# Performance work log

Measured on AMD Instinct MI355X. Metric: run time of the kernel, lower is better.

## Reference

```python
import jax, jax.numpy as jnp
import numpy as np

# SNN constants (standard STBP / quantized-SNN settings used in this style of repo)
THRESH = 0.5   # firing threshold
DECAY = 0.2    # membrane decay
LENS = 0.5     # surrogate-gradient window
QK = 4         # fractional bits for Quantize_Spike(0, 4) / QuantLinear

B, S = 128, 1024
VOCAB, EMB, EDIM, H = 50000, 100, 256, 1024  # H = 2 * num_hiddens


def _quant(x, lo, hi, k=QK):
    n = 2.0 ** k
    return jnp.clip(jnp.round(x * n) / n, lo, hi)


def quant_act(x):
    # Quantize_Spike(0, 4): 0 integer bits, 4 fractional bits, nonneg (post-ReLU)
    return _quant(x, 0.0, 1.0 - 2.0 ** (-QK))


def quant_w(w):
    # QuantLinear weight quantization, symmetric fixed-point
    return _quant(w, -(1.0 - 2.0 ** (-QK)), 1.0 - 2.0 ** (-QK))


def setup_inputs() -> dict:
    key = jax.random.key(0)
    ks = jax.random.split(key, 10)
    f = jnp.float32
    return {
        "inputs": jax.random.randint(ks[0], (B, S), 0, VOCAB),
        "emb": jax.random.normal(ks[1], (VOCAB, EMB), f) * 0.1,
        "W1": jax.random.normal(ks[2], (EDIM, EMB), f) * 0.1,
        "b1": jax.random.normal(ks[3], (EDIM,), f) * 0.01,
        "W2": jax.random.normal(ks[4], (H, EDIM), f) * 0.05,
        "b2": jax.random.normal(ks[5], (H,), f) * 0.01,
        "Wr2": jax.random.normal(ks[6], (H, H), f) * 0.02,
        "br2": jax.random.normal(ks[7], (H,), f) * 0.01,
        "W3": jax.random.normal(ks[8], (2, H), f) * 0.05,
        "b3": jax.random.normal(ks[9], (2,), f) * 0.01,
    }


def reference(inputs, emb, W1, b1, W2, b2, Wr2, br2, W3, b3):
    x = emb[inputs]                                  # [B, S, EMB]
    x = jax.nn.relu(jnp.einsum('bse,he->bsh', x, W1) + b1)  # [B, S, EDIM]
    x = quant_act(x)
    qW2 = quant_w(W2)
    qWr2 = quant_w(Wr2)

    def step(carry, xt):
        mem, spike = carry
        mem = mem * DECAY * (1.0 - spike) + xt @ qW2.T + b2 + spike @ qWr2.T + br2
        spike = (mem > THRESH).astype(mem.dtype)
        return (mem, spike), spike

    init = (jnp.zeros((B, H), jnp.float32), jnp.zeros((B, H), jnp.float32))
    _, spikes = jax.lax.scan(step, init, jnp.transpose(x, (1, 0, 2)))  # [S, B, H]
    sumspike = spikes.sum(axis=0)                    # [B, H]
    return sumspike @ W3.T + b3                      # [B, 2]
```

## Files before the change

kernel.cpp:

```cpp
#include <hip/hip_runtime.h>
#include <stdint.h>

typedef unsigned short u16;
typedef unsigned int   u32;
typedef unsigned char  u8;
typedef signed char    s8;

#define B_    128
#define S_    1024
#define H_    1024
#define E_    256
#define EMB_  100
#define EMBP_ 128
#define V_    50000
#define NTOK_ (B_*S_)
#define FSINF 0x7F7F7F7F

typedef __attribute__((ext_vector_type(8))) short bf16x8;
typedef __attribute__((ext_vector_type(4))) float f32x4;
typedef __attribute__((ext_vector_type(4))) int   i32x4;

__device__ __forceinline__ u16 f2bf(float f){ u32 x=__float_as_uint(f); return (u16)((x + 0x7FFFu + ((x>>16)&1u))>>16); }
__device__ __forceinline__ float quantw(float w){ float r = rintf(w*16.f)*0.0625f; return fminf(fmaxf(r,-0.9375f),0.9375f); }

__device__ __forceinline__ void gll16(const void* g, void* l){
  __builtin_amdgcn_global_load_lds((const __attribute__((address_space(1))) void*)g,
                                   (__attribute__((address_space(3))) void*)l, 16, 0, 0);
}


__global__ __launch_bounds__(256) void prep_all_k(const float* __restrict__ emb,
    const float* __restrict__ W1, const float* __restrict__ W2,
    const float* __restrict__ b2, const float* __restrict__ br2,
    u16* __restrict__ embhi, u16* __restrict__ w1hi, s8* __restrict__ qW2i,
    float* __restrict__ b2br2)
{
  int j = blockIdx.x*256 + threadIdx.x;
  const int N0 = V_*EMBP_;
  const int N1 = E_*EMBP_;
  const int N2 = H_*E_;
  const int N3 = H_;
  if (j < N0){
    int v = j >> 7, k = j & 127;
    embhi[j] = f2bf((k < EMB_) ? emb[v*EMB_ + k] : 0.f);
  } else if ((j -= N0) < N1){
    int n = j >> 7, k = j & 127;
    w1hi[j] = f2bf((k < EMB_) ? W1[n*EMB_ + k] : 0.f);
  } else if ((j -= N1) < N2){
    float q = rintf(W2[j]*16.f);
    qW2i[j] = (s8)(int)fminf(fmaxf(q, -15.f), 15.f);
  } else if ((j -= N2) < N3){
    b2br2[j] = b2[j] + br2[j];
  }
}


__global__ __launch_bounds__(256) void gemm1_k(const int* __restrict__ inputs,
    const u16* __restrict__ embhi, const u16* __restrict__ w1hi,
    const float* __restrict__ b1, u8* __restrict__ xq)
{
  __shared__ __align__(16) char As[16384];
  __shared__ __align__(16) char Bs[16384];
  const int tid = threadIdx.x;
  const int bx = blockIdx.x;
  const int n0 = ((bx >> 3) & 1) * 128;
  const int m0 = (((bx & 7) << 7) + (bx >> 4)) * 128;
  const int l = tid & 63, wid = tid >> 6;
  const int wm = wid >> 1, wn = wid & 1;

  f32x4 acc[4][4];
  #pragma unroll
  for (int a = 0; a < 4; ++a)
    #pragma unroll
    for (int c = 0; c < 4; ++c)
      acc[a][c] = (f32x4)0.f;

  #pragma unroll
  for (int st = 0; st < 2; ++st){
    #pragma unroll
    for (int i = 0; i < 4; ++i){
      int p = tid + i*256, r = p >> 3, c = p & 7;
      int sw = st*128 + ((c ^ (r & 7)) * 16);
      long ga = (long)inputs[m0 + r];
      gll16((const char*)embhi + ga*256 + sw, As + p*16);
      gll16((const char*)w1hi + (long)(n0 + r)*256 + sw, Bs + p*16);
    }
    __syncthreads();
    bf16x8 af[2][4], bfv[2][4];
    #pragma unroll
    for (int kk = 0; kk < 2; ++kk){
      #pragma unroll
      for (int mi = 0; mi < 4; ++mi){
        int rA = wm*64 + mi*16 + (l & 15);
        af[kk][mi] = *(const bf16x8*)&As[rA*128 + (((kk*4 + (l >> 4)) ^ (rA & 7)) * 16)];
      }
      #pragma unroll
      for (int ni = 0; ni < 4; ++ni){
        int rB = wn*64 + ni*16 + (l & 15);
        bfv[kk][ni] = *(const bf16x8*)&Bs[rB*128 + (((kk*4 + (l >> 4)) ^ (rB & 7)) * 16)];
      }
    }
    #pragma unroll
    for (int kk = 0; kk < 2; ++kk)
      #pragma unroll
      for (int mi = 0; mi < 4; ++mi)
        #pragma unroll
        for (int ni = 0; ni < 4; ++ni)
          acc[mi][ni] = __builtin_amdgcn_mfma_f32_16x16x32_bf16(af[kk][mi], bfv[kk][ni], acc[mi][ni], 0, 0, 0);
    __syncthreads();
  }

  #pragma unroll
  for (int mi = 0; mi < 4; ++mi){
    #pragma unroll
    for (int ni = 0; ni < 4; ++ni){
      int col = n0 + wn*64 + ni*16 + (l & 15);
      float bv = b1[col];
      #pragma unroll
      for (int j = 0; j < 4; ++j){
        int row = m0 + wm*64 + mi*16 + ((l >> 4)*4) + j;
        float v = fmaxf(acc[mi][ni][j] + bv, 0.f);
        int q = (int)rintf(v*16.f);
        q = (q > 15) ? 15 : q;
        xq[(size_t)row*E_ + col] = (u8)q;
      }
    }
  }
}


__global__ __launch_bounds__(256, 2) void gemm2_k(const s8* __restrict__ xq,
    const s8* __restrict__ qW2i, const float* __restrict__ b2br2, int* __restrict__ firstspike)
{
  __shared__ __align__(16) char LB[66560];
  float* carry = (float*)(LB + 65536);

  const int tid = threadIdx.x;
  const int bx  = blockIdx.x;
  const int xcd = bx & 7, idx = bx >> 3;
  const int b   = xcd*16 + (idx >> 3);
  const int n0  = (idx & 7) * 128;
  const int l = tid & 63, wid = tid >> 6;
  const int wm = wid >> 1, wn = wid & 1;

  #pragma unroll
  for (int i = 0; i < 8; ++i){
    int p = tid + i*256, r = p >> 4, g = p & 15;
    gll16(qW2i + (size_t)(n0 + r)*256 + ((g ^ (r & 7))*16), LB + p*16);
  }
  __syncthreads();

  i32x4 bq[4][4];
  #pragma unroll
  for (int ni = 0; ni < 4; ++ni){
    int rB = wn*64 + ni*16 + (l & 15);
    #pragma unroll
    for (int ks = 0; ks < 4; ++ks){
      int g = (ks*4 + (l >> 4)) ^ (rB & 7);
      bq[ni][ks] = *(const i32x4*)&LB[rB*256 + g*16];
    }
  }
  float bias_e[4];
  #pragma unroll
  for (int ni = 0; ni < 4; ++ni)
    bias_e[ni] = b2br2[n0 + wn*64 + ni*16 + (l & 15)];
  if (tid < 128) carry[tid] = 0.f;
  __syncthreads();

  const s8* Ab0 = xq + (size_t)b*S_*E_;
  #pragma unroll
  for (int i = 0; i < 4; ++i){
    int p = tid + i*256, r = p >> 4, g = p & 15;
    gll16(Ab0 + (size_t)r*256 + ((g ^ (r & 7))*16), LB + p*16);
  }
  __syncthreads();

  const int hsc = tid & 127, chunk = tid >> 7;
  const int hx = hsc & 15;
  float mmax = -1e30f;

  for (int s = 0; s < 16; ++s){
    const char* Acur = LB + (s & 1)*16384;
    i32x4 aq[2][4];
    #pragma unroll
    for (int mi = 0; mi < 2; ++mi){
      int rA = wm*32 + mi*16 + (l & 15);
      #pragma unroll
      for (int ks = 0; ks < 4; ++ks){
        int g = (ks*4 + (l >> 4)) ^ (rA & 7);
        aq[mi][ks] = *(const i32x4*)&Acur[rA*256 + g*16];
      }
    }
    if (s < 15){
      const s8* Ab = Ab0 + (size_t)(s + 1)*64*256;
      char* dst = LB + ((s + 1) & 1)*16384;
      #pragma unroll
      for (int i = 0; i < 4; ++i){
        int p = tid + i*256, r = p >> 4, g = p & 15;
        gll16(Ab + (size_t)r*256 + ((g ^ (r & 7))*16), dst + p*16);
      }
    }
    i32x4 acc[2][4];
    #pragma unroll
    for (int mi = 0; mi < 2; ++mi)
      #pragma unroll
      for (int ni = 0; ni < 4; ++ni)
        acc[mi][ni] = (i32x4)0;
    #pragma unroll
    for (int ks = 0; ks < 4; ++ks)
      #pragma unroll
      for (int mi = 0; mi < 2; ++mi)
        #pragma unroll
        for (int ni = 0; ni < 4; ++ni)
          acc[mi][ni] = __builtin_amdgcn_mfma_i32_16x16x64_i8(aq[mi][ks], bq[ni][ks], acc[mi][ni], 0, 0, 0);

    #pragma unroll
    for (int mi = 0; mi < 2; ++mi){
      int g = wm*8 + mi*4 + (l >> 4);
      int gp = g ^ (l & 15);
      #pragma unroll
      for (int ni = 0; ni < 4; ++ni){
        int h = wn*64 + ni*16 + (l & 15);
        f32x4 w;
        #pragma unroll
        for (int jj = 0; jj < 4; ++jj)
          w[jj] = fmaf((float)acc[mi][ni][jj], 0.00390625f, bias_e[ni]);
        *(f32x4*)&LB[32768 + h*256 + gp*16] = w;
      }
    }
    __syncthreads();

    const char* sb = LB + 32768 + hsc*256;
    if (chunk == 0){
      float m = carry[(s & 1)*128 + hsc];
      #pragma unroll
      for (int gi = 0; gi < 8; ++gi){
        f32x4 v = *(const f32x4*)(sb + ((gi ^ hx)*16));
        #pragma unroll
        for (int jj = 0; jj < 4; ++jj){ m = fmaf(m, 0.2f, v[jj]); mmax = fmaxf(mmax, m); }
      }
    } else {
      float m = 0.f;
      #pragma unroll
      for (int gi = 4; gi < 8; ++gi){
        f32x4 v = *(const f32x4*)(sb + ((gi ^ hx)*16));
        #pragma unroll
        for (int jj = 0; jj < 4; ++jj) m = fmaf(m, 0.2f, v[jj]);
      }
      #pragma unroll
      for (int gi = 8; gi < 16; ++gi){
        f32x4 v = *(const f32x4*)(sb + ((gi ^ hx)*16));
        #pragma unroll
        for (int jj = 0; jj < 4; ++jj){ m = fmaf(m, 0.2f, v[jj]); mmax = fmaxf(mmax, m); }
      }
      carry[((s + 1) & 1)*128 + hsc] = m;
    }
    __syncthreads();
  }
  if (mmax > 0.5f) atomicMin(&firstspike[b], 0);
}


__global__ __launch_bounds__(256) void fallback_k(const s8* __restrict__ xq, const s8* __restrict__ qW2i,
    const float* __restrict__ b2br2, const float* __restrict__ Wr2,
    const int* __restrict__ firstspike, float* __restrict__ sumspike)
{
  const int b = blockIdx.x;
  if (firstspike[b] >= S_) return;
  const int tid = threadIdx.x;
  __shared__ int slist[H_];
  __shared__ int scount;
  __shared__ s8 xrow[E_];
  float mem[4] = {0,0,0,0}, sp[4] = {0,0,0,0}, ss[4] = {0,0,0,0};

  for (int t = 0; t < S_; ++t){
    if (tid == 0) scount = 0;
    __syncthreads();
    #pragma unroll
    for (int j = 0; j < 4; ++j)
      if (sp[j] > 0.5f){ int k = atomicAdd(&scount, 1); slist[k] = tid + j*256; }
    if (tid < 64) ((int*)xrow)[tid] = ((const int*)(xq + (size_t)(b*S_ + t)*E_))[tid];
    __syncthreads();
    int sc = scount;
    #pragma unroll
    for (int j = 0; j < 4; ++j){
      int h = tid + j*256;
      const s8* wr = qW2i + (size_t)h*E_;
      int ia = 0;
      #pragma unroll 4
      for (int k = 0; k < E_; k += 4){
        ia += (int)xrow[k]*(int)wr[k] + (int)xrow[k+1]*(int)wr[k+1]
            + (int)xrow[k+2]*(int)wr[k+2] + (int)xrow[k+3]*(int)wr[k+3];
      }
      float Iv = (float)ia*(1.f/256.f) + b2br2[h];
      float rec = 0.f;
      for (int u = 0; u < sc; ++u) rec += quantw(Wr2[(size_t)h*H_ + slist[u]]);
      mem[j] = mem[j]*0.2f*(1.f - sp[j]) + Iv + rec;
    }
    #pragma unroll
    for (int j = 0; j < 4; ++j){ float ns = (mem[j] > 0.5f) ? 1.f : 0.f; sp[j] = ns; ss[j] += ns; }
    __syncthreads();
  }
  #pragma unroll
  for (int j = 0; j < 4; ++j)
    sumspike[((size_t)b << 10) + tid + j*256] = ss[j];
}


__global__ __launch_bounds__(256) void final_k(const float* __restrict__ ss, const float* __restrict__ W3,
    const float* __restrict__ b3, float* __restrict__ out)
{
  int b = blockIdx.x, tid = threadIdx.x;
  float p0 = 0.f, p1 = 0.f;
  for (int h = tid; h < H_; h += 256){
    float s = ss[((size_t)b << 10) + h];
    p0 += s*W3[h]; p1 += s*W3[H_ + h];
  }
  #pragma unroll
  for (int o = 32; o > 0; o >>= 1){ p0 += __shfl_down(p0, o, 64); p1 += __shfl_down(p1, o, 64); }
  __shared__ float r0[4], r1[4];
  if ((tid & 63) == 0){ r0[tid >> 6] = p0; r1[tid >> 6] = p1; }
  __syncthreads();
  if (tid == 0){
    out[b*2 + 0] = r0[0] + r0[1] + r0[2] + r0[3] + b3[0];
    out[b*2 + 1] = r1[0] + r1[1] + r1[2] + r1[3] + b3[1];
  }
}


extern "C" void kernel_launch(void* const* d_in, const int* in_sizes, int n_in,
                              void* d_out, int out_size, void* d_ws, size_t ws_size,
                              hipStream_t stream)
{
  (void)in_sizes; (void)n_in; (void)out_size; (void)ws_size;
  const int*   inputs = (const int*)  d_in[0];
  const float* emb    = (const float*)d_in[1];
  const float* W1     = (const float*)d_in[2];
  const float* b1     = (const float*)d_in[3];
  const float* W2     = (const float*)d_in[4];
  const float* b2     = (const float*)d_in[5];
  const float* Wr2    = (const float*)d_in[6];
  const float* br2    = (const float*)d_in[7];
  const float* W3     = (const float*)d_in[8];
  const float* b3     = (const float*)d_in[9];
  float* out = (float*)d_out;
  char* ws = (char*)d_ws;

  size_t off = 0;
  auto alloc = [&](size_t bytes)->char*{
    char* p = ws + off; off = (off + bytes + 255) & ~(size_t)255; return p;
  };
  u16*   embhi    = (u16*)  alloc((size_t)V_*EMBP_*2);
  u16*   w1hi     = (u16*)  alloc((size_t)E_*EMBP_*2);
  s8*    qW2i     = (s8*)   alloc((size_t)H_*E_);
  float* b2br2    = (float*)alloc((size_t)H_*4);
  u8*    xq       = (u8*)   alloc((size_t)NTOK_*E_);
  float* sumspike = (float*)alloc((size_t)B_*H_*4);
  int*   firstspk = (int*)  alloc((size_t)B_*4);

  hipMemsetAsync(sumspike, 0,    (size_t)B_*H_*4, stream);
  hipMemsetAsync(firstspk, 0x7F, (size_t)B_*4,    stream);

  {
    const int total = V_*EMBP_ + E_*EMBP_ + H_*E_ + H_;
    prep_all_k<<<(total + 255)/256, 256, 0, stream>>>(emb, W1, W2, b2, br2,
                                                      embhi, w1hi, qW2i, b2br2);
  }
  gemm1_k<<<2048, 256, 0, stream>>>(inputs, embhi, w1hi, b1, xq);
  gemm2_k<<<1024, 256, 0, stream>>>((const s8*)xq, qW2i, b2br2, firstspk);
  fallback_k<<<B_, 256, 0, stream>>>((const s8*)xq, qW2i, b2br2, Wr2, firstspk, sumspike);
  final_k<<<B_, 256, 0, stream>>>(sumspike, W3, b3, out);
}
```

Baseline: 165.9 us.

## Shrink gemm2 LDS with bf16 staging for 4 blocks/CU; prefetch gemm1 K-stage

In gemm2, the per-step pre-activation tile is staged in LDS as bf16 instead of fp32, and the A tile drops from double to single buffering. This roughly halves LDS use so launch bounds can rise from 2 to 4 blocks per CU, with A fragments now loaded per k-slice right next to the MFMAs. gemm1 prefetches its second K half into registers while the first half computes. Both kernels raise wave priority around the MFMA blocks. The bf16 rounding of membrane inputs could shift threshold-crossing detection near the 0.5 boundary, and single buffering exposes more global-load latency.

```diff
diff --git a/kernel.cpp b/kernel.cpp
--- a/kernel.cpp
+++ b/kernel.cpp
@@ -55,6 +55,34 @@
 }
 
 
+__device__ __forceinline__ void g1_step(const char* As, const char* Bs, f32x4 (&acc)[4][4],
+                                        int wm, int wn, int l)
+{
+  bf16x8 af[2][4], bfv[2][4];
+  #pragma unroll
+  for (int kk = 0; kk < 2; ++kk){
+    #pragma unroll
+    for (int mi = 0; mi < 4; ++mi){
+      int rA = wm*64 + mi*16 + (l & 15);
+      af[kk][mi] = *(const bf16x8*)&As[rA*128 + (((kk*4 + (l >> 4)) ^ (rA & 7)) * 16)];
+    }
+    #pragma unroll
+    for (int ni = 0; ni < 4; ++ni){
+      int rB = wn*64 + ni*16 + (l & 15);
+      bfv[kk][ni] = *(const bf16x8*)&Bs[rB*128 + (((kk*4 + (l >> 4)) ^ (rB & 7)) * 16)];
+    }
+  }
+  __builtin_amdgcn_s_setprio(1);
+  #pragma unroll
+  for (int kk = 0; kk < 2; ++kk)
+    #pragma unroll
+    for (int mi = 0; mi < 4; ++mi)
+      #pragma unroll
+      for (int ni = 0; ni < 4; ++ni)
+        acc[mi][ni] = __builtin_amdgcn_mfma_f32_16x16x32_bf16(af[kk][mi], bfv[kk][ni], acc[mi][ni], 0, 0, 0);
+  __builtin_amdgcn_s_setprio(0);
+}
+
 __global__ __launch_bounds__(256) void gemm1_k(const int* __restrict__ inputs,
     const u16* __restrict__ embhi, const u16* __restrict__ w1hi,
     const float* __restrict__ b1, u8* __restrict__ xq)
@@ -75,40 +103,37 @@
     for (int c = 0; c < 4; ++c)
       acc[a][c] = (f32x4)0.f;
 
-  #pragma unroll
-  for (int st = 0; st < 2; ++st){
-    #pragma unroll
-    for (int i = 0; i < 4; ++i){
-      int p = tid + i*256, r = p >> 3, c = p & 7;
-      int sw = st*128 + ((c ^ (r & 7)) * 16);
-      long ga = (long)inputs[m0 + r];
-      gll16((const char*)embhi + ga*256 + sw, As + p*16);
-      gll16((const char*)w1hi + (long)(n0 + r)*256 + sw, Bs + p*16);
-    }
-    __syncthreads();
-    bf16x8 af[2][4], bfv[2][4];
-    #pragma unroll
-    for (int kk = 0; kk < 2; ++kk){
-      #pragma unroll
-      for (int mi = 0; mi < 4; ++mi){
-        int rA = wm*64 + mi*16 + (l & 15);
-        af[kk][mi] = *(const bf16x8*)&As[rA*128 + (((kk*4 + (l >> 4)) ^ (rA & 7)) * 16)];
-      }
-      #pragma unroll
-      for (int ni = 0; ni < 4; ++ni){
-        int rB = wn*64 + ni*16 + (l & 15);
-        bfv[kk][ni] = *(const bf16x8*)&Bs[rB*128 + (((kk*4 + (l >> 4)) ^ (rB & 7)) * 16)];
-      }
-    }
-    #pragma unroll
-    for (int kk = 0; kk < 2; ++kk)
-      #pragma unroll
-      for (int mi = 0; mi < 4; ++mi)
-        #pragma unroll
-        for (int ni = 0; ni < 4; ++ni)
-          acc[mi][ni] = __builtin_amdgcn_mfma_f32_16x16x32_bf16(af[kk][mi], bfv[kk][ni], acc[mi][ni], 0, 0, 0);
-    __syncthreads();
-  }
+  int ga4[4];
+  #pragma unroll
+  for (int i = 0; i < 4; ++i){
+    int p = tid + i*256, r = p >> 3, c = p & 7;
+    ga4[i] = inputs[m0 + r];
+    int sw = (c ^ (r & 7)) * 16;
+    gll16((const char*)embhi + (size_t)ga4[i]*256 + sw, As + p*16);
+    gll16((const char*)w1hi + (size_t)(n0 + r)*256 + sw, Bs + p*16);
+  }
+  i32x4 pfA[4], pfB[4];
+  #pragma unroll
+  for (int q = 0; q < 4; ++q){
+    int p = tid + q*256, r = p >> 3, c = p & 7;
+    int sw = 128 + ((c ^ (r & 7)) * 16);
+    pfA[q] = *(const i32x4*)((const char*)embhi + (size_t)ga4[q]*256 + sw);
+    pfB[q] = *(const i32x4*)((const char*)w1hi + (size_t)(n0 + r)*256 + sw);
+  }
+  __syncthreads();
+
+  g1_step(As, Bs, acc, wm, wn, l);
+  __syncthreads();
+
+  #pragma unroll
+  for (int q = 0; q < 4; ++q){
+    int p = tid + q*256;
+    *(i32x4*)(As + p*16) = pfA[q];
+    *(i32x4*)(Bs + p*16) = pfB[q];
+  }
+  __syncthreads();
+
+  g1_step(As, Bs, acc, wm, wn, l);
 
   #pragma unroll
   for (int mi = 0; mi < 4; ++mi){
@@ -129,11 +154,11 @@
 }
 
 
-__global__ __launch_bounds__(256, 2) void gemm2_k(const s8* __restrict__ xq,
+__global__ __launch_bounds__(256, 4) void gemm2_k(const s8* __restrict__ xq,
     const s8* __restrict__ qW2i, const float* __restrict__ b2br2, int* __restrict__ firstspike)
 {
-  __shared__ __align__(16) char LB[66560];
-  float* carry = (float*)(LB + 65536);
+  __shared__ __align__(16) char LB[33792];
+  float* carry = (float*)(LB + 32768);
 
   const int tid = threadIdx.x;
   const int bx  = blockIdx.x;
@@ -142,6 +167,7 @@
   const int n0  = (idx & 7) * 128;
   const int l = tid & 63, wid = tid >> 6;
   const int wm = wid >> 1, wn = wid & 1;
+  const int l4 = l >> 4;
 
   #pragma unroll
   for (int i = 0; i < 8; ++i){
@@ -155,10 +181,8 @@
   for (int ni = 0; ni < 4; ++ni){
     int rB = wn*64 + ni*16 + (l & 15);
     #pragma unroll
-    for (int ks = 0; ks < 4; ++ks){
-      int g = (ks*4 + (l >> 4)) ^ (rB & 7);
-      bq[ni][ks] = *(const i32x4*)&LB[rB*256 + g*16];
-    }
+    for (int ks = 0; ks < 4; ++ks)
+      bq[ni][ks] = *(const i32x4*)&LB[rB*256 + (((ks*4 + l4) ^ (rB & 7))*16)];
   }
   float bias_e[4];
   #pragma unroll
@@ -176,82 +200,98 @@
   __syncthreads();
 
   const int hsc = tid & 127, chunk = tid >> 7;
-  const int hx = hsc & 15;
+  const int hx7 = hsc & 7;
+  const int rA0 = wm*32 + (l & 15), rA1 = rA0 + 16;
   float mmax = -1e30f;
 
   for (int s = 0; s < 16; ++s){
-    const char* Acur = LB + (s & 1)*16384;
-    i32x4 aq[2][4];
+    i32x4 acc[2][4];
+    #pragma unroll
+    for (int mi = 0; mi < 2; ++mi)
+      #pragma unroll
+      for (int ni = 0; ni < 4; ++ni)
+        acc[mi][ni] = (i32x4)0;
+
+    __builtin_amdgcn_s_setprio(1);
+    #pragma unroll
+    for (int ks = 0; ks < 4; ++ks){
+      i32x4 a0 = *(const i32x4*)&LB[rA0*256 + (((ks*4 + l4) ^ (rA0 & 7))*16)];
+      i32x4 a1 = *(const i32x4*)&LB[rA1*256 + (((ks*4 + l4) ^ (rA1 & 7))*16)];
+      #pragma unroll
+      for (int ni = 0; ni < 4; ++ni){
+        acc[0][ni] = __builtin_amdgcn_mfma_i32_16x16x64_i8(a0, bq[ni][ks], acc[0][ni], 0, 0, 0);
+        acc[1][ni] = __builtin_amdgcn_mfma_i32_16x16x64_i8(a1, bq[ni][ks], acc[1][ni], 0, 0, 0);
+      }
+    }
+    __builtin_amdgcn_s_setprio(0);
+
     #pragma unroll
     for (int mi = 0; mi < 2; ++mi){
-      int rA = wm*32 + mi*16 + (l & 15);
-      #pragma unroll
-      for (int ks = 0; ks < 4; ++ks){
-        int g = (ks*4 + (l >> 4)) ^ (rA & 7);
-        aq[mi][ks] = *(const i32x4*)&Acur[rA*256 + g*16];
-      }
-    }
+      int tg = wm*4 + mi*2 + (l4 >> 1);
+      int s8off = (l4 & 1)*8;
+      #pragma unroll
+      for (int ni = 0; ni < 4; ++ni){
+        int h = wn*64 + ni*16 + (l & 15);
+        float v0 = fmaf((float)acc[mi][ni][0], 0.00390625f, bias_e[ni]);
+        float v1 = fmaf((float)acc[mi][ni][1], 0.00390625f, bias_e[ni]);
+        float v2 = fmaf((float)acc[mi][ni][2], 0.00390625f, bias_e[ni]);
+        float v3 = fmaf((float)acc[mi][ni][3], 0.00390625f, bias_e[ni]);
+        u32 w0, w1;
+        asm("v_cvt_pk_bf16_f32 %0, %1, %2" : "=v"(w0) : "v"(v0), "v"(v1));
+        asm("v_cvt_pk_bf16_f32 %0, %1, %2" : "=v"(w1) : "v"(v2), "v"(v3));
+        uint2 wv; wv.x = w0; wv.y = w1;
+        *(uint2*)&LB[16384 + h*128 + ((tg ^ (h & 7))*16) + s8off] = wv;
+      }
+    }
+    __syncthreads();
+
     if (s < 15){
       const s8* Ab = Ab0 + (size_t)(s + 1)*64*256;
-      char* dst = LB + ((s + 1) & 1)*16384;
       #pragma unroll
       for (int i = 0; i < 4; ++i){
         int p = tid + i*256, r = p >> 4, g = p & 15;
-        gll16(Ab + (size_t)r*256 + ((g ^ (r & 7))*16), dst + p*16);
-      }
-    }
-    i32x4 acc[2][4];
-    #pragma unroll
-    for (int mi = 0; mi < 2; ++mi)
-      #pragma unroll
-      for (int ni = 0; ni < 4; ++ni)
-        acc[mi][ni] = (i32x4)0;
-    #pragma unroll
-    for (int ks = 0; ks < 4; ++ks)
-      #pragma unroll
-      for (int mi = 0; mi < 2; ++mi)
-        #pragma unroll
-        for (int ni = 0; ni < 4; ++ni)
-          acc[mi][ni] = __builtin_amdgcn_mfma_i32_16x16x64_i8(aq[mi][ks], bq[ni][ks], acc[mi][ni], 0, 0, 0);
-
-    #pragma unroll
-    for (int mi = 0; mi < 2; ++mi){
-      int g = wm*8 + mi*4 + (l >> 4);
-      int gp = g ^ (l & 15);
-      #pragma unroll
-      for (int ni = 0; ni < 4; ++ni){
-        int h = wn*64 + ni*16 + (l & 15);
-        f32x4 w;
-        #pragma unroll
-        for (int jj = 0; jj < 4; ++jj)
-          w[jj] = fmaf((float)acc[mi][ni][jj], 0.00390625f, bias_e[ni]);
-        *(f32x4*)&LB[32768 + h*256 + gp*16] = w;
-      }
-    }
-    __syncthreads();
-
-    const char* sb = LB + 32768 + hsc*256;
+        gll16(Ab + (size_t)r*256 + ((g ^ (r & 7))*16), LB + p*16);
+      }
+    }
+
+    const char* sb = LB + 16384 + hsc*128;
     if (chunk == 0){
       float m = carry[(s & 1)*128 + hsc];
       #pragma unroll
-      for (int gi = 0; gi < 8; ++gi){
-        f32x4 v = *(const f32x4*)(sb + ((gi ^ hx)*16));
+      for (int tg = 0; tg < 4; ++tg){
+        uint4 w = *(const uint4*)(sb + ((tg ^ hx7)*16));
+        const u32* wp = (const u32*)&w;
         #pragma unroll
-        for (int jj = 0; jj < 4; ++jj){ m = fmaf(m, 0.2f, v[jj]); mmax = fmaxf(mmax, m); }
+        for (int j = 0; j < 4; ++j){
+          m = fmaf(m, 0.2f, __uint_as_float(wp[j] << 16));
+          float m2 = fmaf(m, 0.2f, __uint_as_float(wp[j] & 0xFFFF0000u));
+          mmax = fmaxf(fmaxf(mmax, m), m2);
+          m = m2;
+        }
       }
     } else {
       float m = 0.f;
       #pragma unroll
-      for (int gi = 4; gi < 8; ++gi){
-        f32x4 v = *(const f32x4*)(sb + ((gi ^ hx)*16));
+      for (int tg = 2; tg < 4; ++tg){
+        uint4 w = *(const uint4*)(sb + ((tg ^ hx7)*16));
+        const u32* wp = (const u32*)&w;
         #pragma unroll
-        for (int jj = 0; jj < 4; ++jj) m = fmaf(m, 0.2f, v[jj]);
-      }
-      #pragma unroll
-      for (int gi = 8; gi < 16; ++gi){
-        f32x4 v = *(const f32x4*)(sb + ((gi ^ hx)*16));
+        for (int j = 0; j < 4; ++j){
+          m = fmaf(m, 0.2f, __uint_as_float(wp[j] << 16));
+          m = fmaf(m, 0.2f, __uint_as_float(wp[j] & 0xFFFF0000u));
+        }
+      }
+      #pragma unroll
+      for (int tg = 4; tg < 8; ++tg){
+        uint4 w = *(const uint4*)(sb + ((tg ^ hx7)*16));
+        const u32* wp = (const u32*)&w;
         #pragma unroll
-        for (int jj = 0; jj < 4; ++jj){ m = fmaf(m, 0.2f, v[jj]); mmax = fmaxf(mmax, m); }
+        for (int j = 0; j < 4; ++j){
+          m = fmaf(m, 0.2f, __uint_as_float(wp[j] << 16));
+          float m2 = fmaf(m, 0.2f, __uint_as_float(wp[j] & 0xFFFF0000u));
+          mmax = fmaxf(fmaxf(mmax, m), m2);
+          m = m2;
+        }
       }
       carry[((s + 1) & 1)*128 + hsc] = m;
     }
```

New measurement: 166.1 us. About the same (+0.1%).

## Replace exact membrane scan with conservative max-current bound; retile gemm1 with register W1

Applied to the files above, without the earlier changes.

The no-spike check in gemm2 no longer writes currents to LDS and runs the serial decay recurrence. Each thread now tracks the maximum integer input current and tests it against a bound: with decay 0.2 the membrane can never exceed 1.25 times that maximum, so a threshold of 0.399 conservatively flags possible spikes and still hands them to the exact fallback. This removes the LDS staging, the extra barrier and the scalar scan, and W2 fragments are now read straight from global memory into registers. gemm1 is retiled to 64-row blocks with W1 held in registers and a single LDS buffer, doubling the grid, and both kernels raise wave priority around their MFMA sections. The bound can route more batches to the slow fallback if currents sit just below 0.4.

```diff
diff --git a/kernel.cpp b/kernel.cpp
--- a/kernel.cpp
+++ b/kernel.cpp
@@ -55,70 +55,69 @@
 }
 
 
-__global__ __launch_bounds__(256) void gemm1_k(const int* __restrict__ inputs,
+__global__ __launch_bounds__(256, 2) void gemm1_k(const int* __restrict__ inputs,
     const u16* __restrict__ embhi, const u16* __restrict__ w1hi,
     const float* __restrict__ b1, u8* __restrict__ xq)
 {
   __shared__ __align__(16) char As[16384];
-  __shared__ __align__(16) char Bs[16384];
   const int tid = threadIdx.x;
   const int bx = blockIdx.x;
   const int n0 = ((bx >> 3) & 1) * 128;
-  const int m0 = (((bx & 7) << 7) + (bx >> 4)) * 128;
+  const int m0 = ((bx & 7)*256 + (bx >> 4)) * 64;
   const int l = tid & 63, wid = tid >> 6;
-  const int wm = wid >> 1, wn = wid & 1;
-
-  f32x4 acc[4][4];
-  #pragma unroll
-  for (int a = 0; a < 4; ++a)
-    #pragma unroll
-    for (int c = 0; c < 4; ++c)
-      acc[a][c] = (f32x4)0.f;
-
-  #pragma unroll
-  for (int st = 0; st < 2; ++st){
-    #pragma unroll
-    for (int i = 0; i < 4; ++i){
-      int p = tid + i*256, r = p >> 3, c = p & 7;
-      int sw = st*128 + ((c ^ (r & 7)) * 16);
-      long ga = (long)inputs[m0 + r];
-      gll16((const char*)embhi + ga*256 + sw, As + p*16);
-      gll16((const char*)w1hi + (long)(n0 + r)*256 + sw, Bs + p*16);
-    }
-    __syncthreads();
-    bf16x8 af[2][4], bfv[2][4];
-    #pragma unroll
-    for (int kk = 0; kk < 2; ++kk){
-      #pragma unroll
-      for (int mi = 0; mi < 4; ++mi){
-        int rA = wm*64 + mi*16 + (l & 15);
-        af[kk][mi] = *(const bf16x8*)&As[rA*128 + (((kk*4 + (l >> 4)) ^ (rA & 7)) * 16)];
-      }
-      #pragma unroll
-      for (int ni = 0; ni < 4; ++ni){
-        int rB = wn*64 + ni*16 + (l & 15);
-        bfv[kk][ni] = *(const bf16x8*)&Bs[rB*128 + (((kk*4 + (l >> 4)) ^ (rB & 7)) * 16)];
-      }
-    }
-    #pragma unroll
-    for (int kk = 0; kk < 2; ++kk)
-      #pragma unroll
-      for (int mi = 0; mi < 4; ++mi)
-        #pragma unroll
-        for (int ni = 0; ni < 4; ++ni)
-          acc[mi][ni] = __builtin_amdgcn_mfma_f32_16x16x32_bf16(af[kk][mi], bfv[kk][ni], acc[mi][ni], 0, 0, 0);
-    __syncthreads();
-  }
-
-  #pragma unroll
-  for (int mi = 0; mi < 4; ++mi){
+  const int wm = wid & 1, wn = wid >> 1;
+  const int l4 = l >> 4;
+
+  bf16x8 bfv[4][4];
+  #pragma unroll
+  for (int kk = 0; kk < 4; ++kk)
+    #pragma unroll
+    for (int ni = 0; ni < 4; ++ni){
+      int row = n0 + wn*64 + ni*16 + (l & 15);
+      bfv[kk][ni] = *(const bf16x8*)((const char*)w1hi + (size_t)row*256 + kk*64 + l4*16);
+    }
+
+  #pragma unroll
+  for (int i = 0; i < 4; ++i){
+    int p = tid + i*256, r = p >> 4, g = p & 15;
+    long ga = (long)inputs[m0 + r];
+    gll16((const char*)embhi + ga*256 + ((g ^ (r & 15))*16), As + p*16);
+  }
+  __syncthreads();
+
+  f32x4 acc[2][4];
+  #pragma unroll
+  for (int mi = 0; mi < 2; ++mi)
+    #pragma unroll
+    for (int ni = 0; ni < 4; ++ni)
+      acc[mi][ni] = (f32x4)0.f;
+
+  #pragma unroll
+  for (int kk = 0; kk < 4; ++kk){
+    bf16x8 af[2];
+    #pragma unroll
+    for (int mi = 0; mi < 2; ++mi){
+      int rA = wm*32 + mi*16 + (l & 15);
+      af[mi] = *(const bf16x8*)&As[rA*256 + (((kk*4 + l4) ^ (rA & 15))*16)];
+    }
+    __builtin_amdgcn_s_setprio(1);
+    #pragma unroll
+    for (int mi = 0; mi < 2; ++mi)
+      #pragma unroll
+      for (int ni = 0; ni < 4; ++ni)
+        acc[mi][ni] = __builtin_amdgcn_mfma_f32_16x16x32_bf16(af[mi], bfv[kk][ni], acc[mi][ni], 0, 0, 0);
+    __builtin_amdgcn_s_setprio(0);
+  }
+
+  #pragma unroll
+  for (int mi = 0; mi < 2; ++mi){
     #pragma unroll
     for (int ni = 0; ni < 4; ++ni){
       int col = n0 + wn*64 + ni*16 + (l & 15);
       float bv = b1[col];
       #pragma unroll
       for (int j = 0; j < 4; ++j){
-        int row = m0 + wm*64 + mi*16 + ((l >> 4)*4) + j;
+        int row = m0 + wm*32 + mi*16 + l4*4 + j;
         float v = fmaxf(acc[mi][ni][j] + bv, 0.f);
         int q = (int)rintf(v*16.f);
         q = (q > 15) ? 15 : q;
@@ -132,9 +131,7 @@
 __global__ __launch_bounds__(256, 2) void gemm2_k(const s8* __restrict__ xq,
     const s8* __restrict__ qW2i, const float* __restrict__ b2br2, int* __restrict__ firstspike)
 {
-  __shared__ __align__(16) char LB[66560];
-  float* carry = (float*)(LB + 65536);
-
+  __shared__ __align__(16) char LB[32768];
   const int tid = threadIdx.x;
   const int bx  = blockIdx.x;
   const int xcd = bx & 7, idx = bx >> 3;
@@ -142,122 +139,77 @@
   const int n0  = (idx & 7) * 128;
   const int l = tid & 63, wid = tid >> 6;
   const int wm = wid >> 1, wn = wid & 1;
-
-  #pragma unroll
-  for (int i = 0; i < 8; ++i){
-    int p = tid + i*256, r = p >> 4, g = p & 15;
-    gll16(qW2i + (size_t)(n0 + r)*256 + ((g ^ (r & 7))*16), LB + p*16);
-  }
-  __syncthreads();
+  const int l4 = l >> 4;
 
   i32x4 bq[4][4];
+  float be[4];
   #pragma unroll
   for (int ni = 0; ni < 4; ++ni){
-    int rB = wn*64 + ni*16 + (l & 15);
-    #pragma unroll
-    for (int ks = 0; ks < 4; ++ks){
-      int g = (ks*4 + (l >> 4)) ^ (rB & 7);
-      bq[ni][ks] = *(const i32x4*)&LB[rB*256 + g*16];
-    }
-  }
-  float bias_e[4];
-  #pragma unroll
-  for (int ni = 0; ni < 4; ++ni)
-    bias_e[ni] = b2br2[n0 + wn*64 + ni*16 + (l & 15)];
-  if (tid < 128) carry[tid] = 0.f;
-  __syncthreads();
+    int row = n0 + wn*64 + ni*16 + (l & 15);
+    #pragma unroll
+    for (int ks = 0; ks < 4; ++ks)
+      bq[ni][ks] = *(const i32x4*)(qW2i + (size_t)row*256 + ks*64 + l4*16);
+    be[ni] = b2br2[row];
+  }
 
   const s8* Ab0 = xq + (size_t)b*S_*E_;
   #pragma unroll
   for (int i = 0; i < 4; ++i){
     int p = tid + i*256, r = p >> 4, g = p & 15;
-    gll16(Ab0 + (size_t)r*256 + ((g ^ (r & 7))*16), LB + p*16);
+    gll16(Ab0 + (size_t)r*256 + ((g ^ (r & 15))*16), LB + p*16);
   }
   __syncthreads();
 
-  const int hsc = tid & 127, chunk = tid >> 7;
-  const int hx = hsc & 15;
-  float mmax = -1e30f;
+  const int rA0 = wm*32 + (l & 15), rA1 = rA0 + 16;
+  int rmax[4] = {(int)0x80000000, (int)0x80000000, (int)0x80000000, (int)0x80000000};
 
   for (int s = 0; s < 16; ++s){
-    const char* Acur = LB + (s & 1)*16384;
-    i32x4 aq[2][4];
-    #pragma unroll
-    for (int mi = 0; mi < 2; ++mi){
-      int rA = wm*32 + mi*16 + (l & 15);
-      #pragma unroll
-      for (int ks = 0; ks < 4; ++ks){
-        int g = (ks*4 + (l >> 4)) ^ (rA & 7);
-        aq[mi][ks] = *(const i32x4*)&Acur[rA*256 + g*16];
-      }
-    }
     if (s < 15){
       const s8* Ab = Ab0 + (size_t)(s + 1)*64*256;
       char* dst = LB + ((s + 1) & 1)*16384;
       #pragma unroll
       for (int i = 0; i < 4; ++i){
         int p = tid + i*256, r = p >> 4, g = p & 15;
-        gll16(Ab + (size_t)r*256 + ((g ^ (r & 7))*16), dst + p*16);
+        gll16(Ab + (size_t)r*256 + ((g ^ (r & 15))*16), dst + p*16);
       }
     }
+    const char* cur = LB + (s & 1)*16384;
     i32x4 acc[2][4];
     #pragma unroll
     for (int mi = 0; mi < 2; ++mi)
       #pragma unroll
       for (int ni = 0; ni < 4; ++ni)
         acc[mi][ni] = (i32x4)0;
-    #pragma unroll
-    for (int ks = 0; ks < 4; ++ks)
+
+    __builtin_amdgcn_s_setprio(1);
+    #pragma unroll
+    for (int ks = 0; ks < 4; ++ks){
+      i32x4 a0 = *(const i32x4*)&cur[rA0*256 + (((ks*4 + l4) ^ (rA0 & 15))*16)];
+      i32x4 a1 = *(const i32x4*)&cur[rA1*256 + (((ks*4 + l4) ^ (rA1 & 15))*16)];
+      #pragma unroll
+      for (int ni = 0; ni < 4; ++ni){
+        acc[0][ni] = __builtin_amdgcn_mfma_i32_16x16x64_i8(a0, bq[ni][ks], acc[0][ni], 0, 0, 0);
+        acc[1][ni] = __builtin_amdgcn_mfma_i32_16x16x64_i8(a1, bq[ni][ks], acc[1][ni], 0, 0, 0);
+      }
+    }
+    __builtin_amdgcn_s_setprio(0);
+
+    #pragma unroll
+    for (int ni = 0; ni < 4; ++ni)
       #pragma unroll
       for (int mi = 0; mi < 2; ++mi)
         #pragma unroll
-        for (int ni = 0; ni < 4; ++ni)
-          acc[mi][ni] = __builtin_amdgcn_mfma_i32_16x16x64_i8(aq[mi][ks], bq[ni][ks], acc[mi][ni], 0, 0, 0);
-
-    #pragma unroll
-    for (int mi = 0; mi < 2; ++mi){
-      int g = wm*8 + mi*4 + (l >> 4);
-      int gp = g ^ (l & 15);
-      #pragma unroll
-      for (int ni = 0; ni < 4; ++ni){
-        int h = wn*64 + ni*16 + (l & 15);
-        f32x4 w;
-        #pragma unroll
-        for (int jj = 0; jj < 4; ++jj)
-          w[jj] = fmaf((float)acc[mi][ni][jj], 0.00390625f, bias_e[ni]);
-        *(f32x4*)&LB[32768 + h*256 + gp*16] = w;
-      }
-    }
+        for (int j = 0; j < 4; ++j)
+          rmax[ni] = max(rmax[ni], acc[mi][ni][j]);
+
     __syncthreads();
-
-    const char* sb = LB + 32768 + hsc*256;
-    if (chunk == 0){
-      float m = carry[(s & 1)*128 + hsc];
-      #pragma unroll
-      for (int gi = 0; gi < 8; ++gi){
-        f32x4 v = *(const f32x4*)(sb + ((gi ^ hx)*16));
-        #pragma unroll
-        for (int jj = 0; jj < 4; ++jj){ m = fmaf(m, 0.2f, v[jj]); mmax = fmaxf(mmax, m); }
-      }
-    } else {
-      float m = 0.f;
-      #pragma unroll
-      for (int gi = 4; gi < 8; ++gi){
-        f32x4 v = *(const f32x4*)(sb + ((gi ^ hx)*16));
-        #pragma unroll
-        for (int jj = 0; jj < 4; ++jj) m = fmaf(m, 0.2f, v[jj]);
-      }
-      #pragma unroll
-      for (int gi = 8; gi < 16; ++gi){
-        f32x4 v = *(const f32x4*)(sb + ((gi ^ hx)*16));
-        #pragma unroll
-        for (int jj = 0; jj < 4; ++jj){ m = fmaf(m, 0.2f, v[jj]); mmax = fmaxf(mmax, m); }
-      }
-      carry[((s + 1) & 1)*128 + hsc] = m;
-    }
-    __syncthreads();
-  }
-  if (mmax > 0.5f) atomicMin(&firstspike[b], 0);
+  }
+
+  bool trip = false;
+  #pragma unroll
+  for (int ni = 0; ni < 4; ++ni)
+    trip = trip || ((float)rmax[ni]*0.00390625f + be[ni] > 0.399f);
+  if (trip) atomicMin(&firstspike[b], 0);
 }
 
 
@@ -366,7 +318,7 @@
     prep_all_k<<<(total + 255)/256, 256, 0, stream>>>(emb, W1, W2, b2, br2,
                                                       embhi, w1hi, qW2i, b2br2);
   }
-  gemm1_k<<<2048, 256, 0, stream>>>(inputs, embhi, w1hi, b1, xq);
+  gemm1_k<<<4096, 256, 0, stream>>>(inputs, embhi, w1hi, b1, xq);
   gemm2_k<<<1024, 256, 0, stream>>>((const s8*)xq, qW2i, b2br2, firstspk);
   fallback_k<<<B_, 256, 0, stream>>>((const s8*)xq, qW2i, b2br2, Wr2, firstspk, sumspike);
   final_k<<<B_, 256, 0, stream>>>(sumspike, W3, b3, out);
```

Result: slower. 170.5 us (+2.8%).
